# Performance work log

Hardware: AMD Instinct MI355X
Metric: run time of the kernel (lower is better)

Reference implementation:

```python
import jax, jax.numpy as jnp
import numpy as np

# Sizes (must match setup_inputs)
N = 1024      # total residues (2 structures x 512)
B = 2         # num_structid
RPS = 512     # residues per sample
P = 32        # n_protein_patches
E_AB = B * P * P
E_ab = 131072 # downsampled residue-residue edges
DIM = 256
PDIM = 128
NB = 15       # distance RBF basis count
EPS = 1e-6


def _fourier(x, f):
    # GaussianFourierEncoding1D: x [..., 1], f [m] -> [..., 2m]
    ang = 2.0 * jnp.pi * x * f
    return jnp.concatenate([jnp.sin(ang), jnp.cos(ang)], axis=-1)


def _gelu_mlp(x, w1, b1, w2, b2):
    return jnp.dot(jax.nn.gelu(jnp.dot(x, w1) + b1), w2) + b2


def _frames(coords):
    # get_frame_matrix from N, CA, C atoms via Gram-Schmidt; coords [N,3,3]
    a, b, c = coords[:, 0], coords[:, 1], coords[:, 2]
    v1 = c - b
    v2 = a - b
    e1 = v1 / (jnp.linalg.norm(v1, axis=-1, keepdims=True) + EPS)
    u2 = v2 - e1 * jnp.sum(e1 * v2, axis=-1, keepdims=True)
    e2 = u2 / (jnp.linalg.norm(u2, axis=-1, keepdims=True) + EPS)
    e3 = jnp.cross(e1, e2)
    R = jnp.stack([e1, e2, e3], axis=-1)  # columns are the frame axes
    return R, b


def setup_inputs() -> dict:
    key = jax.random.key(0)
    ks = jax.random.split(key, 16)

    def lin(k, i, o):
        return (jax.random.normal(k, (i, o), jnp.float32) / np.sqrt(i)).astype(jnp.float32)

    # per-sample index offsets so gathers stay within each structure
    off_ab = (jnp.arange(E_ab) // (E_ab // B)).astype(jnp.int32) * RPS
    gather_idx_ab_a = jax.random.randint(ks[0], (E_ab,), 0, RPS, jnp.int32) + off_ab
    gather_idx_ab_b = jax.random.randint(ks[1], (E_ab,), 0, RPS, jnp.int32) + off_ab
    off_pid = (jnp.arange(B * P) // P).astype(jnp.int32) * RPS
    gather_idx_pid_a = jax.random.randint(ks[2], (B * P,), 0, RPS, jnp.int32) + off_pid

    return {
        "res_embedding_in": jax.random.normal(ks[3], (N, DIM), jnp.float32),
        "timestep_encoding_prot": jax.random.uniform(ks[4], (N, 1), jnp.float32),
        "input_protein_coords": jax.random.normal(ks[5], (N, 3, 3), jnp.float32) * 3.0,
        "time_freq": jax.random.normal(ks[6], (16,), jnp.float32),
        "chain_freq": jax.random.normal(ks[7], (PDIM // 4,), jnp.float32),
        "w1_res": lin(ks[8], DIM + 32, DIM),
        "b1_res": jnp.zeros((DIM,), jnp.float32),
        "w2_res": lin(ks[9], DIM, DIM),
        "b2_res": jnp.zeros((DIM,), jnp.float32),
        "w_geom": lin(ks[10], NB + 9 + 3, PDIM),
        "w1_edge": lin(ks[11], PDIM + PDIM // 2 + 2 * DIM, DIM),
        "b1_edge": jnp.zeros((DIM,), jnp.float32),
        "w2_edge": lin(ks[12], DIM, PDIM),
        "b2_edge": jnp.zeros((PDIM,), jnp.float32),
        "residue_index": (jnp.arange(N, dtype=jnp.int32) % 256),
        "res_chain_id": (jnp.arange(N, dtype=jnp.int32) // 256),
        "gather_idx_ab_a": gather_idx_ab_a,
        "gather_idx_ab_b": gather_idx_ab_b,
        "gather_idx_pid_a": gather_idx_pid_a,
    }


def reference(res_embedding_in, timestep_encoding_prot, input_protein_coords,
              time_freq, chain_freq,
              w1_res, b1_res, w2_res, b2_res,
              w_geom,
              w1_edge, b1_edge, w2_edge, b2_edge,
              residue_index, res_chain_id,
              gather_idx_ab_a, gather_idx_ab_b, gather_idx_pid_a):
    # residue representation: res_in_mlp(cat(emb, time_enc)) + emb
    te = _fourier(timestep_encoding_prot, time_freq)  # [N, 32]
    rep = _gelu_mlp(jnp.concatenate([res_embedding_in, te], axis=-1),
                    w1_res, b1_res, w2_res, b2_res) + res_embedding_in

    # patch-grid (AB) edge expansion, then merged edge list (ab first, AB second)
    pid = gather_idx_pid_a.reshape(B, P)
    AB_a = jnp.broadcast_to(pid[:, :, None], (B, P, P)).reshape(-1)
    AB_b = jnp.broadcast_to(pid[:, None, :], (B, P, P)).reshape(-1)
    src = jnp.concatenate([gather_idx_ab_a, AB_a])
    dst = jnp.concatenate([gather_idx_ab_b, AB_b])

    # chain relative positional encoding (_compute_chain_pe)
    ri = residue_index.astype(jnp.float32)
    disp = (ri[src] - ri[dst]) / 8.0                        # [E]
    rope = _fourier(disp[:, None], chain_freq) / (jnp.abs(disp) + 1.0)[:, None]
    rope = rope * (res_chain_id[src] == res_chain_id[dst])[:, None]  # [E, PDIM//2]

    # relative geometry encoding from backbone frames
    R, t = _frames(input_protein_coords)
    d = t[dst] - t[src]                                     # [E, 3]
    dist = jnp.sqrt(jnp.sum(d * d, axis=-1) + EPS)
    local = jnp.einsum('eik,ei->ek', R[src], d) / (dist + 1.0)[:, None]
    relrot = jnp.einsum('eia,eib->eab', R[src], R[dst]).reshape(-1, 9)
    centers = jnp.linspace(0.0, 20.0, NB)
    sig = 20.0 / NB
    rbf = jnp.exp(-0.5 * ((dist[:, None] - centers) / sig) ** 2)
    geom = jnp.dot(jnp.concatenate([rbf, relrot, local], axis=-1), w_geom)  # [E, PDIM]

    # pp_edge_embed(cat(geom, chain_pe, rep[src], rep[dst]))
    edge_in = jnp.concatenate([geom, rope, rep[src], rep[dst]], axis=-1)
    edge_reps = _gelu_mlp(edge_in, w1_edge, b1_edge, w2_edge, b2_edge)  # [E, PDIM]
    return edge_reps
```

## Files before the change

kernel.cpp:

```cpp
#include <hip/hip_runtime.h>


typedef __attribute__((ext_vector_type(8))) short short8;
typedef __attribute__((ext_vector_type(4))) float f32x4;

#define TWO_PI 6.283185307179586f
#define E_AB_TOT 131072

#define WS_RT    0
#define WS_REPB  49152
#define WS_W1F   573440
#define WS_W2F   884736
#define WS_PS    950272
#define WS_PD    1998848

__device__ __forceinline__ unsigned short f2bf(float x){
  unsigned int u = __float_as_uint(x);
  u += 0x7fffu + ((u >> 16) & 1u);
  return (unsigned short)(u >> 16);
}

__device__ __forceinline__ unsigned int pack_bf16(float lo, float hi){
  unsigned int ul = __float_as_uint(lo), uh = __float_as_uint(hi);
  ul += 0x7fffu + ((ul >> 16) & 1u);
  uh += 0x7fffu + ((uh >> 16) & 1u);
  return __builtin_amdgcn_perm(uh, ul, 0x07060302);
}

__device__ __forceinline__ float gelu_s(float x){
  float s = x * x;
  float w = x * __builtin_fmaf(-0.1029437f, s, -2.30220847f);
  float e = __builtin_exp2f(w);
  return x * __builtin_amdgcn_rcpf(1.0f + e);
}

__global__ __launch_bounds__(256) void prep_k(
    const float* __restrict__ emb, const float* __restrict__ ts,
    const float* __restrict__ tf,  const float* __restrict__ w1,
    const float* __restrict__ b1,  const float* __restrict__ w2,
    const float* __restrict__ b2,  unsigned short* __restrict__ repb,
    const float* __restrict__ coords, float* __restrict__ RT,
    const float* __restrict__ wg, const float* __restrict__ w1e,
    unsigned short* __restrict__ w1f,
    const float* __restrict__ w2e, unsigned short* __restrict__ w2f){
  __shared__ float xt[288 * 12];
  __shared__ float ht[256 * 12];
  int blk = blockIdx.x, tid = threadIdx.x;
  if (blk < 128){
    int n0 = blk * 8;
    #pragma unroll
    for (int nd = 0; nd < 8; ++nd)
      xt[tid * 12 + nd] = emb[(n0 + nd) * 256 + tid];
    {
      int nd = tid >> 5, j = tid & 31;
      float ang = TWO_PI * ts[n0 + nd] * tf[j & 15];
      float s, c; __sincosf(ang, &s, &c);
      xt[(256 + j) * 12 + nd] = (j < 16) ? s : c;
    }
    __syncthreads();
    float acc[8];
    float bias1 = b1[tid];
    #pragma unroll
    for (int nd = 0; nd < 8; ++nd) acc[nd] = bias1;
    #pragma unroll 4
    for (int k = 0; k < 288; ++k){
      float w = w1[k * 256 + tid];
      f32x4 xa = *(const f32x4*)&xt[k * 12];
      f32x4 xb = *(const f32x4*)&xt[k * 12 + 4];
      acc[0] += xa[0]*w; acc[1] += xa[1]*w; acc[2] += xa[2]*w; acc[3] += xa[3]*w;
      acc[4] += xb[0]*w; acc[5] += xb[1]*w; acc[6] += xb[2]*w; acc[7] += xb[3]*w;
    }
    #pragma unroll
    for (int nd = 0; nd < 8; ++nd) ht[tid * 12 + nd] = gelu_s(acc[nd]);
    __syncthreads();
    float acc2[8];
    float bias2 = b2[tid];
    #pragma unroll
    for (int nd = 0; nd < 8; ++nd) acc2[nd] = bias2;
    #pragma unroll 4
    for (int k = 0; k < 256; ++k){
      float w = w2[k * 256 + tid];
      f32x4 ha = *(const f32x4*)&ht[k * 12];
      f32x4 hb = *(const f32x4*)&ht[k * 12 + 4];
      acc2[0] += ha[0]*w; acc2[1] += ha[1]*w; acc2[2] += ha[2]*w; acc2[3] += ha[3]*w;
      acc2[4] += hb[0]*w; acc2[5] += hb[1]*w; acc2[6] += hb[2]*w; acc2[7] += hb[3]*w;
    }
    #pragma unroll
    for (int nd = 0; nd < 8; ++nd)
      repb[(n0 + nd) * 256 + tid] = f2bf(acc2[nd] + xt[tid * 12 + nd]);
  } else if (blk < 132){
    int n = (blk - 128) * 256 + tid;
    const float* p = coords + n * 9;
    float ax=p[0],ay=p[1],az=p[2], bx=p[3],by=p[4],bz=p[5], cx=p[6],cy=p[7],cz=p[8];
    float v1x=cx-bx, v1y=cy-by, v1z=cz-bz;
    float v2x=ax-bx, v2y=ay-by, v2z=az-bz;
    float n1 = sqrtf(v1x*v1x+v1y*v1y+v1z*v1z) + 1e-6f;
    float e1x=v1x/n1, e1y=v1y/n1, e1z=v1z/n1;
    float dp = e1x*v2x + e1y*v2y + e1z*v2z;
    float u2x=v2x-e1x*dp, u2y=v2y-e1y*dp, u2z=v2z-e1z*dp;
    float n2 = sqrtf(u2x*u2x+u2y*u2y+u2z*u2z) + 1e-6f;
    float e2x=u2x/n2, e2y=u2y/n2, e2z=u2z/n2;
    float* r = RT + n * 12;
    r[0]=e1x; r[1]=e2x; r[2]=e1y*e2z - e1z*e2y;
    r[3]=e1y; r[4]=e2y; r[5]=e1z*e2x - e1x*e2z;
    r[6]=e1z; r[7]=e2z; r[8]=e1x*e2y - e1y*e2x;
    r[9]=bx;  r[10]=by; r[11]=bz;
  } else if (blk < 148){
    int u = (blk - 132) * 4 + (tid >> 6);
    int lane = tid & 63;
    int s = u >> 3, c = u & 7;
    int n  = c * 16 + (lane & 15);
    int kb = s * 32 + (lane >> 4) * 8;
    unsigned short* o = w2f + (((s * 8 + c) * 64) + lane) * 8;
    unsigned short vals[8];
    #pragma unroll
    for (int j = 0; j < 8; ++j)
      vals[j] = f2bf(w2e[(kb + j) * 128 + n]);
    *(uint4*)o = *(const uint4*)vals;
  } else {
    int u = (blk - 148) * 4 + (tid >> 6);
    int lane = tid & 63;
    int s = u >> 4, c = u & 15;
    int n  = c * 16 + (lane & 15);
    int kb = s * 32 + (lane >> 4) * 8;
    unsigned short* o = w1f + (((s * 16 + c) * 64) + lane) * 8;
    unsigned short vals[8];
    for (int j = 0; j < 8; ++j){
      int k = kb + j;
      float val;
      if (k < 27){
        val = 0.f;
        for (int j2 = 0; j2 < 128; ++j2) val += wg[k * 128 + j2] * w1e[j2 * 256 + n];
      }
      else if (k < 91)  val = w1e[(128 + k - 27)  * 256 + n];
      else if (k < 96)  val = 0.f;
      else if (k < 352) val = w1e[(192 + k - 96)  * 256 + n];
      else              val = w1e[(448 + k - 352) * 256 + n];
      vals[j] = f2bf(val);
    }
    *(uint4*)o = *(const uint4*)vals;
  }
}

__global__ __launch_bounds__(512) void proj_k(
    const unsigned short* __restrict__ repb,
    const unsigned short* __restrict__ w1f,
    const float* __restrict__ b1e,
    float* __restrict__ ps, float* __restrict__ pd)
{
  int part = blockIdx.x & 1;
  int nt   = blockIdx.x >> 1;
  int tid  = threadIdx.x, w = tid >> 6, lane = tid & 63;
  int c0 = w * 2, lr = lane & 15, quad = lane >> 4;
  int n0g = nt * 64;
  const short8* w1f8 = (const short8*)w1f;
  f32x4 acc[8];
  #pragma unroll
  for (int i = 0; i < 8; ++i) acc[i] = (f32x4){0.f, 0.f, 0.f, 0.f};
  int sb = 3 + part * 8;
  #pragma unroll
  for (int s = 0; s < 8; ++s){
    short8 a0 = w1f8[((sb + s) * 16 + c0 + 0) * 64 + lane];
    short8 a1 = w1f8[((sb + s) * 16 + c0 + 1) * 64 + lane];
    #pragma unroll
    for (int t = 0; t < 4; ++t){
      short8 b = *(const short8*)(repb + (n0g + t * 16 + lr) * 256 + s * 32 + quad * 8);
      acc[t]     = __builtin_amdgcn_mfma_f32_16x16x32_bf16(a0, b, acc[t],     0, 0, 0);
      acc[4 + t] = __builtin_amdgcn_mfma_f32_16x16x32_bf16(a1, b, acc[4 + t], 0, 0, 0);
    }
  }
  float* out = part ? pd : ps;
  #pragma unroll
  for (int c = 0; c < 2; ++c){
    int n = (c0 + c) * 16 + quad * 4;
    f32x4 add = (f32x4){0.f, 0.f, 0.f, 0.f};
    if (!part) add = *(const f32x4*)(b1e + n);
    #pragma unroll
    for (int t = 0; t < 4; ++t){
      f32x4 v = acc[c * 4 + t];
      v[0] += add[0]; v[1] += add[1]; v[2] += add[2]; v[3] += add[3];
      *(f32x4*)(out + (n0g + t * 16 + lr) * 256 + n) = v;
    }
  }
}

__global__ __launch_bounds__(512, 4) void edge_k(
    const float* __restrict__ RT,  const float* __restrict__ cf,
    const int* __restrict__ resi, const int* __restrict__ chain,
    const int* __restrict__ gia,  const int* __restrict__ gib,
    const int* __restrict__ pid,
    const unsigned short* __restrict__ w1f, const unsigned short* __restrict__ w2f,
    const float* __restrict__ ps, const float* __restrict__ pd,
    const float* __restrict__ bias2,
    float* __restrict__ outp)
{
  __shared__ __align__(16) char smem[35840];
  __shared__ __align__(16) float rtbuf[128][12];
  __shared__ float scD[64];
  __shared__ float scI[64];
  __shared__ int lsrc[64];
  __shared__ int ldst[64];

  int tid = threadIdx.x;
  int e0  = blockIdx.x * 64;

  if (tid < 64){
    int e = e0 + tid, s_, d_;
    if (e < E_AB_TOT){ s_ = gia[e]; d_ = gib[e]; }
    else {
      int i = e - E_AB_TOT;
      int b = i >> 10, w_ = i & 1023;
      s_ = pid[b * 32 + (w_ >> 5)];
      d_ = pid[b * 32 + (w_ & 31)];
    }
    lsrc[tid] = s_; ldst[tid] = d_;
    float disp = ((float)resi[s_] - (float)resi[d_]) * 0.125f;
    scD[tid] = disp;
    scI[tid] = (chain[s_] == chain[d_]) ? 1.f / (fabsf(disp) + 1.f) : 0.f;
  } else if (tid < 192){
    int r  = tid - 64;
    int e  = e0 + (r & 63);
    int node;
    if (e < E_AB_TOT){ node = (r < 64) ? gia[e] : gib[e]; }
    else {
      int i = e - E_AB_TOT;
      int b = i >> 10, w_ = i & 1023;
      node = (r < 64) ? pid[b * 32 + (w_ >> 5)] : pid[b * 32 + (w_ & 31)];
    }
    const f32x4* p = (const f32x4*)(RT + node * 12);
    f32x4* q = (f32x4*)(&rtbuf[r][0]);
    q[0] = p[0]; q[1] = p[1]; q[2] = p[2];
  }
  __syncthreads();

  {
    #pragma unroll
    for (int it = 0; it < 4; ++it){
      int v = it * 512 + tid, ed = v >> 5, j = v & 31;
      float ang = TWO_PI * scD[ed] * cf[j];
      float s, c; __sincosf(ang, &s, &c);
      float inv = scI[ed];
      unsigned short* row = (unsigned short*)(smem + ed * 208);
      row[27 + j] = f2bf(s * inv);
      row[59 + j] = f2bf(c * inv);
    }
    #pragma unroll
    for (int it = 0; it < 2; ++it){
      int v = it * 512 + tid, ed = v >> 4, c = v & 15;
      float tx = rtbuf[64 + ed][9]  - rtbuf[ed][9];
      float ty = rtbuf[64 + ed][10] - rtbuf[ed][10];
      float tz = rtbuf[64 + ed][11] - rtbuf[ed][11];
      float dist = sqrtf(tx*tx + ty*ty + tz*tz + 1e-6f);
      if (c < 15){
        float z = (dist - (float)c * (20.f / 14.f)) * (15.f / 20.f);
        ((unsigned short*)(smem + ed * 208))[c] = f2bf(__expf(-0.5f * z * z));
      }
    }
    #pragma unroll
    for (int it = 0; it < 2; ++it){
      int v = it * 512 + tid, ed = v >> 4, cc = v & 15;
      if (cc < 12){
        const float* Rs = &rtbuf[ed][0];
        const float* Rd = &rtbuf[64 + ed][0];
        float val;
        if (cc < 9){
          int a  = (cc >= 6) ? 2 : ((cc >= 3) ? 1 : 0);
          int b_ = cc - 3 * a;
          val = Rs[a]*Rd[b_] + Rs[3+a]*Rd[3+b_] + Rs[6+a]*Rd[6+b_];
        } else {
          int k = cc - 9;
          float tx = Rd[9]-Rs[9], ty = Rd[10]-Rs[10], tz = Rd[11]-Rs[11];
          float dist = sqrtf(tx*tx + ty*ty + tz*tz + 1e-6f);
          val = (Rs[k]*tx + Rs[3+k]*ty + Rs[6+k]*tz) / (dist + 1.f);
        }
        ((unsigned short*)(smem + ed * 208))[15 + cc] = f2bf(val);
      }
    }
    {
      int ed = tid >> 3, c8 = tid & 7;
      ((unsigned short*)(smem + ed * 208))[91 + c8] = 0;
    }
  }
  __syncthreads();

  int w    = tid >> 6, lane = tid & 63;
  int c0   = w * 2;
  int lr   = lane & 15;
  int quad = lane >> 4, qoff = quad * 16;
  f32x4 acc[8];
  #pragma unroll
  for (int i = 0; i < 8; ++i) acc[i] = (f32x4){0.f, 0.f, 0.f, 0.f};
  const short8* w1f8 = (const short8*)w1f;

  #pragma unroll
  for (int s = 0; s < 3; ++s){
    short8 a0 = w1f8[(s * 16 + c0 + 0) * 64 + lane];
    short8 a1 = w1f8[(s * 16 + c0 + 1) * 64 + lane];
    short8 be0 = *(const short8*)(smem + ( 0 + lr) * 208 + s * 64 + qoff);
    short8 be1 = *(const short8*)(smem + (16 + lr) * 208 + s * 64 + qoff);
    short8 be2 = *(const short8*)(smem + (32 + lr) * 208 + s * 64 + qoff);
    short8 be3 = *(const short8*)(smem + (48 + lr) * 208 + s * 64 + qoff);
    acc[0] = __builtin_amdgcn_mfma_f32_16x16x32_bf16(a0, be0, acc[0], 0, 0, 0);
    acc[1] = __builtin_amdgcn_mfma_f32_16x16x32_bf16(a0, be1, acc[1], 0, 0, 0);
    acc[2] = __builtin_amdgcn_mfma_f32_16x16x32_bf16(a0, be2, acc[2], 0, 0, 0);
    acc[3] = __builtin_amdgcn_mfma_f32_16x16x32_bf16(a0, be3, acc[3], 0, 0, 0);
    acc[4] = __builtin_amdgcn_mfma_f32_16x16x32_bf16(a1, be0, acc[4], 0, 0, 0);
    acc[5] = __builtin_amdgcn_mfma_f32_16x16x32_bf16(a1, be1, acc[5], 0, 0, 0);
    acc[6] = __builtin_amdgcn_mfma_f32_16x16x32_bf16(a1, be2, acc[6], 0, 0, 0);
    acc[7] = __builtin_amdgcn_mfma_f32_16x16x32_bf16(a1, be3, acc[7], 0, 0, 0);
  }
  __syncthreads();

  {
    char* Hb = smem;
    #pragma unroll
    for (int c = 0; c < 2; ++c){
      int n = (c0 + c) * 16 + quad * 4;
      f32x4 pv[4], qv[4];
      #pragma unroll
      for (int t = 0; t < 4; ++t){
        pv[t] = *(const f32x4*)(ps + (size_t)lsrc[t * 16 + lr] * 256 + n);
        qv[t] = *(const f32x4*)(pd + (size_t)ldst[t * 16 + lr] * 256 + n);
      }
      #pragma unroll
      for (int t = 0; t < 4; ++t){
        int e = t * 16 + lr;
        f32x4 s4 = acc[c * 4 + t];
        float v0 = gelu_s(s4[0] + pv[t][0] + qv[t][0]);
        float v1 = gelu_s(s4[1] + pv[t][1] + qv[t][1]);
        float v2 = gelu_s(s4[2] + pv[t][2] + qv[t][2]);
        float v3 = gelu_s(s4[3] + pv[t][3] + qv[t][3]);
        uint2 p; p.x = pack_bf16(v0, v1); p.y = pack_bf16(v2, v3);
        *(uint2*)(Hb + e * 560 + n * 2) = p;
      }
    }
  }
  __syncthreads();

  int c2 = (w & 3) * 2;
  int eb = (w >> 2) * 32;
  f32x4 acc2[4];
  #pragma unroll
  for (int i = 0; i < 4; ++i) acc2[i] = (f32x4){0.f, 0.f, 0.f, 0.f};
  const short8* w2f8 = (const short8*)w2f;
  #pragma unroll
  for (int s = 0; s < 8; ++s){
    short8 aa0 = w2f8[(s * 8 + c2 + 0) * 64 + lane];
    short8 aa1 = w2f8[(s * 8 + c2 + 1) * 64 + lane];
    short8 h0 = *(const short8*)(smem + (eb +  0 + lr) * 560 + s * 64 + qoff);
    short8 h1 = *(const short8*)(smem + (eb + 16 + lr) * 560 + s * 64 + qoff);
    acc2[0] = __builtin_amdgcn_mfma_f32_16x16x32_bf16(aa0, h0, acc2[0], 0, 0, 0);
    acc2[1] = __builtin_amdgcn_mfma_f32_16x16x32_bf16(aa0, h1, acc2[1], 0, 0, 0);
    acc2[2] = __builtin_amdgcn_mfma_f32_16x16x32_bf16(aa1, h0, acc2[2], 0, 0, 0);
    acc2[3] = __builtin_amdgcn_mfma_f32_16x16x32_bf16(aa1, h1, acc2[3], 0, 0, 0);
  }

  {
    int n0 = c2 * 16 + quad * 4;
    f32x4 bz0 = *(const f32x4*)(bias2 + n0);
    f32x4 bz1 = *(const f32x4*)(bias2 + n0 + 16);
    float* og = outp + (size_t)e0 * 128;
    #pragma unroll
    for (int t = 0; t < 2; ++t){
      int e = eb + t * 16 + lr;
      f32x4 v0, v1;
      v0[0] = acc2[t][0] + bz0[0]; v0[1] = acc2[t][1] + bz0[1];
      v0[2] = acc2[t][2] + bz0[2]; v0[3] = acc2[t][3] + bz0[3];
      v1[0] = acc2[2 + t][0] + bz1[0]; v1[1] = acc2[2 + t][1] + bz1[1];
      v1[2] = acc2[2 + t][2] + bz1[2]; v1[3] = acc2[2 + t][3] + bz1[3];
      *(f32x4*)(og + (size_t)e * 128 + n0)      = v0;
      *(f32x4*)(og + (size_t)e * 128 + n0 + 16) = v1;
    }
  }
}

extern "C" void kernel_launch(void* const* d_in, const int* in_sizes, int n_in,
                              void* d_out, int out_size, void* d_ws, size_t ws_size,
                              hipStream_t stream) {
  const float* emb    = (const float*)d_in[0];
  const float* ts     = (const float*)d_in[1];
  const float* coords = (const float*)d_in[2];
  const float* tf     = (const float*)d_in[3];
  const float* cf     = (const float*)d_in[4];
  const float* w1r    = (const float*)d_in[5];
  const float* b1r    = (const float*)d_in[6];
  const float* w2r    = (const float*)d_in[7];
  const float* b2r    = (const float*)d_in[8];
  const float* wg     = (const float*)d_in[9];
  const float* w1e    = (const float*)d_in[10];
  const float* b1e    = (const float*)d_in[11];
  const float* w2e    = (const float*)d_in[12];
  const float* b2e    = (const float*)d_in[13];
  const int* resi     = (const int*)d_in[14];
  const int* chain    = (const int*)d_in[15];
  const int* gia      = (const int*)d_in[16];
  const int* gib      = (const int*)d_in[17];
  const int* pid      = (const int*)d_in[18];

  char* ws = (char*)d_ws;
  float* RT            = (float*)(ws + WS_RT);
  unsigned short* REPB = (unsigned short*)(ws + WS_REPB);
  unsigned short* W1F  = (unsigned short*)(ws + WS_W1F);
  unsigned short* W2F  = (unsigned short*)(ws + WS_W2F);
  float* PS            = (float*)(ws + WS_PS);
  float* PD            = (float*)(ws + WS_PD);
  float* outp          = (float*)d_out;

  hipLaunchKernelGGL(prep_k, dim3(224), dim3(256), 0, stream,
                     emb, ts, tf, w1r, b1r, w2r, b2r, REPB,
                     coords, RT, wg, w1e, W1F, w2e, W2F);
  hipLaunchKernelGGL(proj_k, dim3(32), dim3(512), 0, stream,
                     REPB, W1F, b1e, PS, PD);
  hipLaunchKernelGGL(edge_k, dim3(2080), dim3(512), 0, stream,
                     RT, cf, resi, chain, gia, gib, pid, W1F, W2F, PS, PD,
                     b2e, outp);
}
```

Measured before the change: 218.4 us.

## Parallelize geometry weight fold, swizzle hidden smem, permute projection layout, raise occupancy

The w_geom x w1_edge fold (27 rows x 128 inner) moves out of the serial per-thread loop into dedicated prep blocks that stage w1e slabs in shared memory. Proj blocks then pack those folded rows into the bf16 fragment layout. PS/PD are stored in a per-wave permuted column order so edge_k's gathers read 32 contiguous bytes per lane. The hidden tile uses an XOR-swizzled 512-byte row stride instead of 560-byte padding, which shrinks shared memory so launch bounds can ask for 8 blocks per SM. The risks are register pressure from the higher occupancy target and an extra dependency between the prep and proj kernels.

```diff
diff --git a/kernel.cpp b/kernel.cpp
--- a/kernel.cpp
+++ b/kernel.cpp
@@ -13,6 +13,7 @@
 #define WS_W2F   884736
 #define WS_PS    950272
 #define WS_PD    1998848
+#define WS_WG1   3047424
 
 __device__ __forceinline__ unsigned short f2bf(float x){
   unsigned int u = __float_as_uint(x);
@@ -42,7 +43,8 @@
     const float* __restrict__ coords, float* __restrict__ RT,
     const float* __restrict__ wg, const float* __restrict__ w1e,
     unsigned short* __restrict__ w1f,
-    const float* __restrict__ w2e, unsigned short* __restrict__ w2f){
+    const float* __restrict__ w2e, unsigned short* __restrict__ w2f,
+    float* __restrict__ wg1){
   __shared__ float xt[288 * 12];
   __shared__ float ht[256 * 12];
   int blk = blockIdx.x, tid = threadIdx.x;
@@ -117,8 +119,8 @@
     for (int j = 0; j < 8; ++j)
       vals[j] = f2bf(w2e[(kb + j) * 128 + n]);
     *(uint4*)o = *(const uint4*)vals;
-  } else {
-    int u = (blk - 148) * 4 + (tid >> 6);
+  } else if (blk < 220){
+    int u = 16 + (blk - 148) * 4 + (tid >> 6);
     int lane = tid & 63;
     int s = u >> 4, c = u & 15;
     int n  = c * 16 + (lane & 15);
@@ -128,26 +130,60 @@
     for (int j = 0; j < 8; ++j){
       int k = kb + j;
       float val;
-      if (k < 27){
-        val = 0.f;
-        for (int j2 = 0; j2 < 128; ++j2) val += wg[k * 128 + j2] * w1e[j2 * 256 + n];
-      }
-      else if (k < 91)  val = w1e[(128 + k - 27)  * 256 + n];
+      if (k < 91)       val = w1e[(128 + k - 27)  * 256 + n];
       else if (k < 96)  val = 0.f;
       else if (k < 352) val = w1e[(192 + k - 96)  * 256 + n];
       else              val = w1e[(448 + k - 352) * 256 + n];
       vals[j] = f2bf(val);
     }
     *(uint4*)o = *(const uint4*)vals;
+  } else {
+    int b2_ = blk - 220;
+    int n0 = b2_ * 16;
+    float* slab = xt;
+    #pragma unroll
+    for (int i = 0; i < 8; ++i){
+      int idx = tid + 256 * i;
+      slab[idx] = w1e[(idx >> 4) * 256 + n0 + (idx & 15)];
+    }
+    __syncthreads();
+    #pragma unroll
+    for (int i = 0; i < 2; ++i){
+      int o = tid + 256 * i;
+      if (o < 432){
+        int k = o >> 4, c = o & 15;
+        float acc = 0.f;
+        for (int j2 = 0; j2 < 128; ++j2)
+          acc += wg[k * 128 + j2] * slab[j2 * 16 + c];
+        wg1[k * 256 + n0 + c] = acc;
+      }
+    }
   }
 }
 
 __global__ __launch_bounds__(512) void proj_k(
     const unsigned short* __restrict__ repb,
-    const unsigned short* __restrict__ w1f,
-    const float* __restrict__ b1e,
+    unsigned short* __restrict__ w1f,
+    const float* __restrict__ b1e, const float* __restrict__ wg1,
+    const float* __restrict__ w1e,
     float* __restrict__ ps, float* __restrict__ pd)
 {
+  if (blockIdx.x >= 32){
+    int u = (blockIdx.x - 32) * 8 + (threadIdx.x >> 6);
+    int lane = threadIdx.x & 63;
+    int n  = u * 16 + (lane & 15);
+    int kb = (lane >> 4) * 8;
+    unsigned short* o = w1f + ((u * 64) + lane) * 8;
+    unsigned short vals[8];
+    #pragma unroll
+    for (int j = 0; j < 8; ++j){
+      int k = kb + j;
+      float val = (k < 27) ? wg1[k * 256 + n] : w1e[(128 + k - 27) * 256 + n];
+      vals[j] = f2bf(val);
+    }
+    *(uint4*)o = *(const uint4*)vals;
+    return;
+  }
   int part = blockIdx.x & 1;
   int nt   = blockIdx.x >> 1;
   int tid  = threadIdx.x, w = tid >> 6, lane = tid & 63;
@@ -172,19 +208,18 @@
   float* out = part ? pd : ps;
   #pragma unroll
   for (int c = 0; c < 2; ++c){
-    int n = (c0 + c) * 16 + quad * 4;
     f32x4 add = (f32x4){0.f, 0.f, 0.f, 0.f};
-    if (!part) add = *(const f32x4*)(b1e + n);
+    if (!part) add = *(const f32x4*)(b1e + (c0 + c) * 16 + quad * 4);
     #pragma unroll
     for (int t = 0; t < 4; ++t){
       f32x4 v = acc[c * 4 + t];
       v[0] += add[0]; v[1] += add[1]; v[2] += add[2]; v[3] += add[3];
-      *(f32x4*)(out + (n0g + t * 16 + lr) * 256 + n) = v;
-    }
-  }
-}
-
-__global__ __launch_bounds__(512, 4) void edge_k(
+      *(f32x4*)(out + (n0g + t * 16 + lr) * 256 + w * 32 + quad * 8 + c * 4) = v;
+    }
+  }
+}
+
+__global__ __launch_bounds__(512, 8) void edge_k(
     const float* __restrict__ RT,  const float* __restrict__ cf,
     const int* __restrict__ resi, const int* __restrict__ chain,
     const int* __restrict__ gia,  const int* __restrict__ gib,
@@ -194,7 +229,7 @@
     const float* __restrict__ bias2,
     float* __restrict__ outp)
 {
-  __shared__ __align__(16) char smem[35840];
+  __shared__ __align__(16) char smem[32768];
   __shared__ __align__(16) float rtbuf[128][12];
   __shared__ float scD[64];
   __shared__ float scI[64];
@@ -309,19 +344,26 @@
     acc[6] = __builtin_amdgcn_mfma_f32_16x16x32_bf16(a1, be2, acc[6], 0, 0, 0);
     acc[7] = __builtin_amdgcn_mfma_f32_16x16x32_bf16(a1, be3, acc[7], 0, 0, 0);
   }
+
+  int offS[4], offD[4];
+  #pragma unroll
+  for (int t = 0; t < 4; ++t){
+    offS[t] = lsrc[t * 16 + lr] * 256 + w * 32 + quad * 8;
+    offD[t] = ldst[t * 16 + lr] * 256 + w * 32 + quad * 8;
+  }
   __syncthreads();
 
   {
     char* Hb = smem;
     #pragma unroll
     for (int c = 0; c < 2; ++c){
-      int n = (c0 + c) * 16 + quad * 4;
       f32x4 pv[4], qv[4];
       #pragma unroll
       for (int t = 0; t < 4; ++t){
-        pv[t] = *(const f32x4*)(ps + (size_t)lsrc[t * 16 + lr] * 256 + n);
-        qv[t] = *(const f32x4*)(pd + (size_t)ldst[t * 16 + lr] * 256 + n);
+        pv[t] = *(const f32x4*)(ps + offS[t] + c * 4);
+        qv[t] = *(const f32x4*)(pd + offD[t] + c * 4);
       }
+      int n = (c0 + c) * 16 + quad * 4;
       #pragma unroll
       for (int t = 0; t < 4; ++t){
         int e = t * 16 + lr;
@@ -331,7 +373,7 @@
         float v2 = gelu_s(s4[2] + pv[t][2] + qv[t][2]);
         float v3 = gelu_s(s4[3] + pv[t][3] + qv[t][3]);
         uint2 p; p.x = pack_bf16(v0, v1); p.y = pack_bf16(v2, v3);
-        *(uint2*)(Hb + e * 560 + n * 2) = p;
+        *(uint2*)(Hb + ((e * 512 + n * 2) ^ ((e & 7) << 4))) = p;
       }
     }
   }
@@ -339,6 +381,7 @@
 
   int c2 = (w & 3) * 2;
   int eb = (w >> 2) * 32;
+  int hx = (lr & 7) << 4;
   f32x4 acc2[4];
   #pragma unroll
   for (int i = 0; i < 4; ++i) acc2[i] = (f32x4){0.f, 0.f, 0.f, 0.f};
@@ -347,8 +390,8 @@
   for (int s = 0; s < 8; ++s){
     short8 aa0 = w2f8[(s * 8 + c2 + 0) * 64 + lane];
     short8 aa1 = w2f8[(s * 8 + c2 + 1) * 64 + lane];
-    short8 h0 = *(const short8*)(smem + (eb +  0 + lr) * 560 + s * 64 + qoff);
-    short8 h1 = *(const short8*)(smem + (eb + 16 + lr) * 560 + s * 64 + qoff);
+    short8 h0 = *(const short8*)(smem + (((eb +  0 + lr) * 512 + s * 64 + qoff) ^ hx));
+    short8 h1 = *(const short8*)(smem + (((eb + 16 + lr) * 512 + s * 64 + qoff) ^ hx));
     acc2[0] = __builtin_amdgcn_mfma_f32_16x16x32_bf16(aa0, h0, acc2[0], 0, 0, 0);
     acc2[1] = __builtin_amdgcn_mfma_f32_16x16x32_bf16(aa0, h1, acc2[1], 0, 0, 0);
     acc2[2] = __builtin_amdgcn_mfma_f32_16x16x32_bf16(aa1, h0, acc2[2], 0, 0, 0);
@@ -404,13 +447,14 @@
   unsigned short* W2F  = (unsigned short*)(ws + WS_W2F);
   float* PS            = (float*)(ws + WS_PS);
   float* PD            = (float*)(ws + WS_PD);
+  float* WG1           = (float*)(ws + WS_WG1);
   float* outp          = (float*)d_out;
 
-  hipLaunchKernelGGL(prep_k, dim3(224), dim3(256), 0, stream,
+  hipLaunchKernelGGL(prep_k, dim3(236), dim3(256), 0, stream,
                      emb, ts, tf, w1r, b1r, w2r, b2r, REPB,
-                     coords, RT, wg, w1e, W1F, w2e, W2F);
-  hipLaunchKernelGGL(proj_k, dim3(32), dim3(512), 0, stream,
-                     REPB, W1F, b1e, PS, PD);
+                     coords, RT, wg, w1e, W1F, w2e, W2F, WG1);
+  hipLaunchKernelGGL(proj_k, dim3(34), dim3(512), 0, stream,
+                     REPB, W1F, b1e, WG1, w1e, PS, PD);
   hipLaunchKernelGGL(edge_k, dim3(2080), dim3(512), 0, stream,
                      RT, cf, resi, chain, gia, gib, pid, W1F, W2F, PS, PD,
                      b2e, outp);
```

After: 222.6 us. Within noise of the previous version (+1.9%).
